# Kernel optimization log

Hardware: AMD Instinct MI355X
Metric: run time of the kernel (lower is better)

The kernel has to match this reference:

```python
import jax, jax.numpy as jnp
import numpy as np
from jax import lax

N, C, H, W = 64, 96, 18, 32
S_IN = 320          # input_state_size
HEADS, HD = 4, 96 // 4
HID = 96            # HIDDEN_SIZE
ENC = 320           # ENC_SIZE
K = 3               # KERNEL_SIZE


def _conv(x, k, b):
    y = lax.conv_general_dilated(x, k, (1, 1), 'SAME',
                                 dimension_numbers=('NCHW', 'OIHW', 'NCHW'))
    return y + b[None, :, None, None]


def setup_inputs() -> dict:
    key = jax.random.key(0)
    ks = jax.random.split(key, 16)
    sc = 0.02
    inp = {
        'x': jax.random.normal(ks[0], (N, C, H, W), jnp.float32),
        'x_state': jax.random.normal(ks[1], (N, S_IN), jnp.float32),
        'actor_keys': jax.random.randint(ks[2], (N,), 0, N),
        'hidden_states': 0.1 * jax.random.normal(ks[3], (N, HID, H, W), jnp.float32),
        # modulation Linear(S_IN -> 2*C), bias init 0
        'W_mod': sc * jax.random.normal(ks[4], (S_IN, 2 * C), jnp.float32),
        'b_mod': jnp.zeros((2 * C,), jnp.float32),
        # FiLM attention: qkv 1x1 proj and output proj
        'W_qkv': sc * jax.random.normal(ks[5], (C, 3 * C), jnp.float32),
        'b_qkv': jnp.zeros((3 * C,), jnp.float32),
        'W_proj': sc * jax.random.normal(ks[6], (C, C), jnp.float32),
        'b_proj': jnp.zeros((C,), jnp.float32),
        # IRConv2dCell (ConvGRU-style): gates conv (2C -> 2*HID), candidate conv (2C -> HID)
        'K_zr': sc * jax.random.normal(ks[7], (2 * HID, 2 * C, K, K), jnp.float32),
        'b_zr': jnp.zeros((2 * HID,), jnp.float32),
        'K_c': sc * jax.random.normal(ks[8], (HID, 2 * C, K, K), jnp.float32),
        'b_c': jnp.zeros((HID,), jnp.float32),
        # PosConv: learned positional map + 1x1 conv to ENC
        'pos_emb': sc * jax.random.normal(ks[9], (1, HID, H, W), jnp.float32),
        'W_pos': sc * jax.random.normal(ks[10], (ENC, HID), jnp.float32),
        'b_pos': jnp.zeros((ENC,), jnp.float32),
    }
    return inp


def reference(x, x_state, actor_keys, hidden_states,
              W_mod, b_mod, W_qkv, b_qkv, W_proj, b_proj,
              K_zr, b_zr, K_c, b_c, pos_emb, W_pos, b_pos):
    HW = H * W
    # modulation -> FiLM params
    mod = x_state @ W_mod + b_mod                       # [N, 2C]
    mm, mb = jnp.split(mod, 2, axis=1)                  # [N, C] each
    # FiLM-conditioned attention over spatial positions
    xm = x * mm[:, :, None, None] + mb[:, :, None, None]  # [N,C,H,W]
    xf = xm.reshape(N, C, HW).transpose(0, 2, 1)          # [N,HW,C]
    qkv = xf @ W_qkv + b_qkv                              # [N,HW,3C]
    q, k, v = jnp.split(qkv, 3, axis=-1)
    q = q.reshape(N, HW, HEADS, HD).transpose(0, 2, 1, 3)  # [N,h,HW,hd]
    k = k.reshape(N, HW, HEADS, HD).transpose(0, 2, 1, 3)
    v = v.reshape(N, HW, HEADS, HD).transpose(0, 2, 1, 3)
    attn = jax.nn.softmax(jnp.einsum('nhqd,nhkd->nhqk', q, k) / np.sqrt(HD), axis=-1)
    o = jnp.einsum('nhqk,nhkd->nhqd', attn, v)            # [N,h,HW,hd]
    o = o.transpose(0, 2, 1, 3).reshape(N, HW, C)
    o = o @ W_proj + b_proj
    y = x + o.transpose(0, 2, 1).reshape(N, C, H, W)      # residual
    # actor-keyed recurrent conv memory cell (gather per actor key)
    h = hidden_states[actor_keys]                         # [N,HID,H,W]
    xh = jnp.concatenate([y, h], axis=1)                  # [N,2C,H,W]
    zr = _conv(xh, K_zr, b_zr)
    z, r = jnp.split(jax.nn.sigmoid(zr), 2, axis=1)
    c = jnp.tanh(_conv(jnp.concatenate([y, r * h], axis=1), K_c, b_c))
    h_new = (1.0 - z) * h + z * c                         # [N,HID,H,W]
    # pooled outputs
    x_visual = h_new.reshape(N, HID, H // 2, 2, W // 2, 2).mean(axis=(3, 5))
    e = h_new + pos_emb
    enc = jnp.einsum('nchw,oc->nohw', e, W_pos) + b_pos[None, :, None, None]
    x_visual_enc = enc.max(axis=(2, 3))                   # [N,ENC]
    return (x_visual, x_visual_enc)
```

## Files before the change

### kernel.cpp

```cpp
#include <hip/hip_runtime.h>
#include <hip/hip_bf16.h>
#include <math.h>

#define NN 64
#define CC 96
#define HH 18
#define WW 32
#define HWP 576
#define SIN 320
#define NHEADS 4
#define HDIM 24
#define HIDC 96
#define ENCC 320

#define MOD_OFF   0
#define A_OFF     12288
#define Y_OFF     (A_OFF)
#define Z_OFF     (A_OFF + 3538944)
#define RH_OFF    (A_OFF + 7077888)
#define O_OFF     (A_OFF + 10616832)
#define HN_OFF    (O_OFF)
#define PART_OFF  (O_OFF + 3538944)
#define WTZR_OFF  (PART_OFF + 163840)
#define WTC_OFF   (WTZR_OFF + 165888)

typedef __attribute__((ext_vector_type(8))) short short8;
typedef __attribute__((ext_vector_type(4))) float f32x4;
typedef __attribute__((ext_vector_type(2))) unsigned int uint2v;
#define MFMA16(a, b, c) __builtin_amdgcn_mfma_f32_16x16x32_bf16(a, b, c, 0, 0, 0)

__device__ inline unsigned short f2bf(float f) {
  __hip_bfloat16 h = __float2bfloat16(f);
  return *reinterpret_cast<unsigned short*>(&h);
}
__device__ inline unsigned int cvtpk(float lo, float hi) {
  unsigned int r;
  asm volatile("v_cvt_pk_bf16_f32 %0, %1, %2" : "=v"(r) : "v"(lo), "v"(hi));
  return r;
}
union S8U { short8 s; unsigned int u[4]; };

__global__ __launch_bounds__(256) void k_modwt(const float* __restrict__ xs,
    const float* __restrict__ Wm, const float* __restrict__ bm,
    float* __restrict__ mod, const float* __restrict__ Kzr,
    const float* __restrict__ Kc, short* __restrict__ wz,
    short* __restrict__ wc) {
  __shared__ float s[SIN];
  int bid = blockIdx.x;
  if (bid < 64) {
    int n = bid;
    for (int i = threadIdx.x; i < SIN; i += 256) s[i] = xs[n * SIN + i];
    __syncthreads();
    int j = threadIdx.x;
    if (j < 192) {
      float acc = bm[j];
      #pragma unroll 4
      for (int k = 0; k < SIN; ++k) acc = fmaf(s[k], Wm[k * 192 + j], acc);
      mod[n * 192 + j] = acc;
    }
  } else {
    int idx = (bid - 64) * 256 + threadIdx.x;
    if (idx < 36864) {
      int oc = idx / 192, ic = idx % 192;
      const float* src = Kzr + (size_t)idx * 9;
      #pragma unroll
      for (int t = 0; t < 9; ++t)
        wz[(t * 192 + oc) * 192 + ic] = (short)f2bf(src[t]);
    } else {
      int j = idx - 36864;
      if (j < 18432) {
        int oc = j / 192, ic = j % 192;
        const float* src = Kc + (size_t)j * 9;
        #pragma unroll
        for (int t = 0; t < 9; ++t)
          wc[(t * 96 + oc) * 192 + ic] = (short)f2bf(src[t]);
      }
    }
  }
}

__global__ __launch_bounds__(256) void k_qkv(const float* __restrict__ x,
    const float* __restrict__ mod, const float* __restrict__ Wq,
    const float* __restrict__ bq, float* __restrict__ qkv) {
  int id = blockIdx.x;
  int n = id & 63, pt = id >> 6;
  int p0 = pt * 96;
  __shared__ __align__(16) short XT[96 * 104];
  int tid = threadIdx.x, lane = tid & 63, wid = tid >> 6;
  int wr = wid >> 1, wcn = wid & 1;
  int cl = lane & 15, kg = lane >> 4;
  #pragma unroll
  for (int w = 0; w < 9; ++w) {
    int lin = tid + 256 * w;
    int cp = lin / 48, pp = (lin % 48) * 2;
    float mA = mod[n * 192 + 2 * cp], bA = mod[n * 192 + 96 + 2 * cp];
    float mB = mod[n * 192 + 2 * cp + 1], bB = mod[n * 192 + 96 + 2 * cp + 1];
    float2 xa = *reinterpret_cast<const float2*>(
        &x[((size_t)n * CC + 2 * cp) * HWP + p0 + pp]);
    float2 xb = *reinterpret_cast<const float2*>(
        &x[((size_t)n * CC + 2 * cp + 1) * HWP + p0 + pp]);
    *reinterpret_cast<unsigned int*>(&XT[pp * 104 + 2 * cp]) =
        cvtpk(fmaf(xa.x, mA, bA), fmaf(xb.x, mB, bB));
    *reinterpret_cast<unsigned int*>(&XT[(pp + 1) * 104 + 2 * cp]) =
        cvtpk(fmaf(xa.y, mA, bA), fmaf(xb.y, mB, bB));
  }
  __syncthreads();

  f32x4 acc[3][9];
  #pragma unroll
  for (int mt = 0; mt < 3; ++mt)
    #pragma unroll
    for (int nt = 0; nt < 9; ++nt) acc[mt][nt] = (f32x4){0.f, 0.f, 0.f, 0.f};

  #pragma unroll
  for (int kc = 0; kc < 3; ++kc) {
    short8 af[3];
    #pragma unroll
    for (int mt = 0; mt < 3; ++mt) {
      int row = wr * 48 + mt * 16 + cl;
      af[mt] = *reinterpret_cast<const short8*>(
          &XT[row * 104 + kc * 32 + kg * 8]);
    }
    #pragma unroll
    for (int nt = 0; nt < 9; ++nt) {
      int j = wcn * 144 + nt * 16 + cl;
      const float* wp = Wq + (size_t)(kc * 32 + kg * 8) * 288 + j;
      S8U b;
      b.u[0] = cvtpk(wp[0], wp[288]);
      b.u[1] = cvtpk(wp[576], wp[864]);
      b.u[2] = cvtpk(wp[1152], wp[1440]);
      b.u[3] = cvtpk(wp[1728], wp[2016]);
      #pragma unroll
      for (int mt = 0; mt < 3; ++mt)
        acc[mt][nt] = MFMA16(af[mt], b.s, acc[mt][nt]);
    }
  }

  #pragma unroll
  for (int nt = 0; nt < 9; ++nt) {
    int j = wcn * 144 + nt * 16 + cl;
    float bias = bq[j];
    #pragma unroll
    for (int mt = 0; mt < 3; ++mt) {
      int pr = p0 + wr * 48 + mt * 16 + kg * 4;
      float* dst = qkv + ((size_t)n * HWP + pr) * 288 + j;
      dst[0] = acc[mt][nt][0] + bias;
      dst[288] = acc[mt][nt][1] + bias;
      dst[576] = acc[mt][nt][2] + bias;
      dst[864] = acc[mt][nt][3] + bias;
    }
  }
}

__global__ __launch_bounds__(256) void k_attn(const float* __restrict__ qkv,
                                              float* __restrict__ o) {
  int id = blockIdx.x;
  int n = id & 63, head = id >> 6;
  __shared__ __align__(16) short K_lds[576 * 40];
  __shared__ __align__(16) short VT_lds[24 * 584];
  __shared__ __align__(16) short P_lds[4 * 144 * 40];
  int tid = threadIdx.x, lane = tid & 63, wid = tid >> 6;
  int cl = lane & 15, kg = lane >> 4;
  const float* base = qkv + (size_t)n * HWP * 288;
  int qoff = head * HDIM, koff = CC + head * HDIM, voff = 2 * CC + head * HDIM;
  const float scale = 0.2041241452319315f;

  for (int p = tid; p < HWP; p += 256) {
    const float* ksrc = base + (size_t)p * 288 + koff;
    #pragma unroll
    for (int g = 0; g < 3; ++g) {
      float4 a = *(const float4*)(ksrc + g * 8);
      float4 b = *(const float4*)(ksrc + g * 8 + 4);
      S8U t;
      t.u[0] = cvtpk(a.x, a.y); t.u[1] = cvtpk(a.z, a.w);
      t.u[2] = cvtpk(b.x, b.y); t.u[3] = cvtpk(b.z, b.w);
      *reinterpret_cast<short8*>(&K_lds[p * 40 + g * 8]) = t.s;
    }
    *reinterpret_cast<short8*>(&K_lds[p * 40 + 24]) =
        (short8){0, 0, 0, 0, 0, 0, 0, 0};
    const float* vsrc = base + (size_t)p * 288 + voff;
    #pragma unroll
    for (int d = 0; d < HDIM; ++d) VT_lds[d * 584 + p] = (short)f2bf(vsrc[d]);
  }

  int qbase = wid * 144;
  short8 qf[9];
  #pragma unroll
  for (int qt = 0; qt < 9; ++qt) {
    if (kg < 3) {
      const float* qs =
          base + (size_t)(qbase + qt * 16 + cl) * 288 + qoff + kg * 8;
      float4 a = *(const float4*)qs;
      float4 b = *(const float4*)(qs + 4);
      S8U t;
      t.u[0] = cvtpk(a.x * scale, a.y * scale);
      t.u[1] = cvtpk(a.z * scale, a.w * scale);
      t.u[2] = cvtpk(b.x * scale, b.y * scale);
      t.u[3] = cvtpk(b.z * scale, b.w * scale);
      qf[qt] = t.s;
    } else {
      qf[qt] = (short8){0, 0, 0, 0, 0, 0, 0, 0};
    }
  }
  __syncthreads();

  f32x4 acc[9][2];
  float m[9], l[9];
  #pragma unroll
  for (int qt = 0; qt < 9; ++qt) {
    acc[qt][0] = (f32x4){0.f, 0.f, 0.f, 0.f};
    acc[qt][1] = (f32x4){0.f, 0.f, 0.f, 0.f};
    m[qt] = -1e30f; l[qt] = 0.f;
  }
  short* pw = P_lds + wid * 5760;
  const f32x4 z4 = (f32x4){0.f, 0.f, 0.f, 0.f};

  for (int ch = 0; ch < 18; ++ch) {
    int key0 = ch * 32;
    short8 ka0 = *reinterpret_cast<const short8*>(
        &K_lds[(key0 + cl) * 40 + kg * 8]);
    short8 ka1 = *reinterpret_cast<const short8*>(
        &K_lds[(key0 + 16 + cl) * 40 + kg * 8]);
    #pragma unroll
    for (int qt = 0; qt < 9; ++qt) {
      f32x4 s0 = MFMA16(ka0, qf[qt], z4);
      f32x4 s1 = MFMA16(ka1, qf[qt], z4);
      float mx = fmaxf(fmaxf(fmaxf(s0[0], s0[1]), fmaxf(s0[2], s0[3])),
                       fmaxf(fmaxf(s1[0], s1[1]), fmaxf(s1[2], s1[3])));
      mx = fmaxf(mx, __shfl_xor(mx, 16));
      mx = fmaxf(mx, __shfl_xor(mx, 32));
      float mn = fmaxf(m[qt], mx);
      float corr = __expf(m[qt] - mn);
      float p0 = __expf(s0[0] - mn), p1 = __expf(s0[1] - mn);
      float p2 = __expf(s0[2] - mn), p3 = __expf(s0[3] - mn);
      float p4 = __expf(s1[0] - mn), p5 = __expf(s1[1] - mn);
      float p6 = __expf(s1[2] - mn), p7 = __expf(s1[3] - mn);
      float sum = ((p0 + p1) + (p2 + p3)) + ((p4 + p5) + (p6 + p7));
      sum += __shfl_xor(sum, 16);
      sum += __shfl_xor(sum, 32);
      l[qt] = l[qt] * corr + sum;
      m[qt] = mn;
      float c0 = __shfl(corr, kg * 4 + 0);
      float c1 = __shfl(corr, kg * 4 + 1);
      float c2 = __shfl(corr, kg * 4 + 2);
      float c3 = __shfl(corr, kg * 4 + 3);
      acc[qt][0][0] *= c0; acc[qt][0][1] *= c1;
      acc[qt][0][2] *= c2; acc[qt][0][3] *= c3;
      acc[qt][1][0] *= c0; acc[qt][1][1] *= c1;
      acc[qt][1][2] *= c2; acc[qt][1][3] *= c3;
      uint2v w0 = {cvtpk(p0, p1), cvtpk(p2, p3)};
      uint2v w1 = {cvtpk(p4, p5), cvtpk(p6, p7)};
      short* prow = pw + (qt * 16 + cl) * 40;
      *reinterpret_cast<uint2v*>(&prow[4 * kg]) = w0;
      *reinterpret_cast<uint2v*>(&prow[16 + 4 * kg]) = w1;
    }
    short8 vb0 = *reinterpret_cast<const short8*>(
        &VT_lds[cl * 584 + key0 + kg * 8]);
    short8 vb1 = (cl < 8) ? *reinterpret_cast<const short8*>(
                                &VT_lds[(16 + cl) * 584 + key0 + kg * 8])
                          : (short8){0, 0, 0, 0, 0, 0, 0, 0};
    #pragma unroll
    for (int qt = 0; qt < 9; ++qt) {
      short8 pa = *reinterpret_cast<const short8*>(
          &pw[(qt * 16 + cl) * 40 + kg * 8]);
      acc[qt][0] = MFMA16(pa, vb0, acc[qt][0]);
      acc[qt][1] = MFMA16(pa, vb1, acc[qt][1]);
    }
  }

  #pragma unroll
  for (int qt = 0; qt < 9; ++qt) {
    float li0 = 1.f / __shfl(l[qt], kg * 4 + 0);
    float li1 = 1.f / __shfl(l[qt], kg * 4 + 1);
    float li2 = 1.f / __shfl(l[qt], kg * 4 + 2);
    float li3 = 1.f / __shfl(l[qt], kg * 4 + 3);
    #pragma unroll
    for (int dt = 0; dt < 2; ++dt) {
      int d = dt * 16 + cl;
      if (dt == 1 && cl >= 8) continue;
      size_t ob = ((size_t)n * HWP + qbase + qt * 16 + kg * 4) * CC
                  + head * HDIM + d;
      o[ob] = acc[qt][dt][0] * li0;
      o[ob + CC] = acc[qt][dt][1] * li1;
      o[ob + 2 * CC] = acc[qt][dt][2] * li2;
      o[ob + 3 * CC] = acc[qt][dt][3] * li3;
    }
  }
}

__global__ __launch_bounds__(256) void k_proj(const float* __restrict__ o,
    const float* __restrict__ Wp, const float* __restrict__ bp,
    const float* __restrict__ x, float* __restrict__ y) {
  int id = blockIdx.x;
  int n = id & 63, pt = id >> 6;
  int p0 = pt * 96;
  __shared__ __align__(16) short XT[96 * 104];
  int tid = threadIdx.x, lane = tid & 63, wid = tid >> 6;
  int wr = wid >> 1, wcn = wid & 1;
  int cl = lane & 15, kg = lane >> 4;
  #pragma unroll
  for (int w = 0; w < 9; ++w) {
    int lin = tid + 256 * w;
    int p = lin / 24, cg = lin % 24;
    float4 v = *reinterpret_cast<const float4*>(
        &o[((size_t)n * HWP + p0 + p) * CC + cg * 4]);
    uint2v u = {cvtpk(v.x, v.y), cvtpk(v.z, v.w)};
    *reinterpret_cast<uint2v*>(&XT[p * 104 + cg * 4]) = u;
  }
  __syncthreads();

  f32x4 acc[3][3];
  #pragma unroll
  for (int mt = 0; mt < 3; ++mt)
    #pragma unroll
    for (int nt = 0; nt < 3; ++nt) acc[mt][nt] = (f32x4){0.f, 0.f, 0.f, 0.f};

  #pragma unroll
  for (int kc = 0; kc < 3; ++kc) {
    short8 af[3];
    #pragma unroll
    for (int mt = 0; mt < 3; ++mt) {
      int row = wr * 48 + mt * 16 + cl;
      af[mt] = *reinterpret_cast<const short8*>(
          &XT[row * 104 + kc * 32 + kg * 8]);
    }
    #pragma unroll
    for (int nt = 0; nt < 3; ++nt) {
      int j = wcn * 48 + nt * 16 + cl;
      const float* wp = Wp + (size_t)(kc * 32 + kg * 8) * 96 + j;
      S8U b;
      b.u[0] = cvtpk(wp[0], wp[96]);
      b.u[1] = cvtpk(wp[192], wp[288]);
      b.u[2] = cvtpk(wp[384], wp[480]);
      b.u[3] = cvtpk(wp[576], wp[672]);
      #pragma unroll
      for (int mt = 0; mt < 3; ++mt)
        acc[mt][nt] = MFMA16(af[mt], b.s, acc[mt][nt]);
    }
  }

  #pragma unroll
  for (int nt = 0; nt < 3; ++nt) {
    int j = wcn * 48 + nt * 16 + cl;
    float bias = bp[j];
    #pragma unroll
    for (int mt = 0; mt < 3; ++mt) {
      int pr = p0 + wr * 48 + mt * 16 + kg * 4;
      size_t yi = ((size_t)n * CC + j) * HWP + pr;
      float4 xv = *reinterpret_cast<const float4*>(&x[yi]);
      float4 o4 = {xv.x + acc[mt][nt][0] + bias, xv.y + acc[mt][nt][1] + bias,
                   xv.z + acc[mt][nt][2] + bias, xv.w + acc[mt][nt][3] + bias};
      *reinterpret_cast<float4*>(&y[yi]) = o4;
    }
  }
}


__global__ __launch_bounds__(256) void k_conv_zr(const float* __restrict__ y,
    const float* __restrict__ hidden, const int* __restrict__ keys,
    const short* __restrict__ wt, const float* __restrict__ bb,
    float* __restrict__ z, float* __restrict__ rh) {
  int id = blockIdx.x;
  int n = id & 63, b = id >> 6;
  int bp = b % 6, bo = b / 6;
  int key = keys[n];
  int ocb = bo * 96;
  __shared__ __align__(16) short XT[170 * 68];
  int tid = threadIdx.x;
  int lane = tid & 63, wid = tid >> 6;
  int wr = wid >> 1, wc = wid & 1;
  int col = lane & 15, kg = lane >> 4;
  int icp = tid >> 4, psub = tid & 15;
  int pg0 = (3 * bp - 1) * 32;
  unsigned int* XTu = reinterpret_cast<unsigned int*>(XT);

  for (int i = tid; i < 5780; i += 256) XTu[i] = 0;

  f32x4 acc[3][3];
  #pragma unroll
  for (int m = 0; m < 3; ++m)
    #pragma unroll
    for (int nt = 0; nt < 3; ++nt) acc[m][nt] = (f32x4){0.f, 0.f, 0.f, 0.f};
  int rowm[3], pxm[3];
  #pragma unroll
  for (int m = 0; m < 3; ++m) {
    int pl = wr * 48 + m * 16 + col;
    rowm[m] = pl >> 5;
    pxm[m] = pl & 31;
  }
  int wl = (ocb + wc * 48 + col) * 192 + kg * 8;
  const float* hsrc = hidden + (size_t)key * HIDC * HWP;
  __syncthreads();

  #pragma unroll
  for (int ph = 0; ph < 3; ++ph) {
    #pragma unroll
    for (int c = 0; c < 2; ++c) {
      int gc = ph * 64 + c * 32;
      const float* s0 = (gc < 96)
          ? y + ((size_t)n * CC + gc + 2 * icp) * HWP
          : hsrc + (size_t)(gc - 96 + 2 * icp) * HWP;
      const float* s1 = s0 + HWP;
      #pragma unroll
      for (int j = 0; j < 5; ++j) {
        int pos = 32 * j + 2 * psub;
        int pg = pg0 + pos;
        bool ok = (pg >= 0 && pg < HWP);
        float2 a = ok ? *reinterpret_cast<const float2*>(s0 + pg)
                      : float2{0.f, 0.f};
        float2 bv = ok ? *reinterpret_cast<const float2*>(s1 + pg)
                       : float2{0.f, 0.f};
        int pidx0 = j * 34 + 1 + 2 * psub;
        XTu[pidx0 * 34 + c * 16 + icp] = cvtpk(a.x, bv.x);
        XTu[(pidx0 + 1) * 34 + c * 16 + icp] = cvtpk(a.y, bv.y);
      }
    }
    __syncthreads();
    #pragma unroll 3
    for (int t = 0; t < 9; ++t) {
      int dyp = t / 3, dxp = t % 3;
      const short* wci = wt + wl + t * 36864 + ph * 64;
      #pragma unroll
      for (int qc = 0; qc < 2; ++qc) {
        short8 b0 = *reinterpret_cast<const short8*>(wci + qc * 32);
        short8 b1 = *reinterpret_cast<const short8*>(wci + qc * 32 + 3072);
        short8 b2 = *reinterpret_cast<const short8*>(wci + qc * 32 + 6144);
        #pragma unroll
        for (int m = 0; m < 3; ++m) {
          int pidx = (rowm[m] + dyp) * 34 + pxm[m] + dxp;
          short8 a = *reinterpret_cast<const short8*>(
              XT + pidx * 68 + qc * 32 + kg * 8);
          acc[m][0] = MFMA16(a, b0, acc[m][0]);
          acc[m][1] = MFMA16(a, b1, acc[m][1]);
          acc[m][2] = MFMA16(a, b2, acc[m][2]);
        }
      }
    }
    __syncthreads();
  }

  #pragma unroll
  for (int nt = 0; nt < 3; ++nt) {
    int oc = ocb + wc * 48 + nt * 16 + col;
    float bias = bb[oc];
    #pragma unroll
    for (int m = 0; m < 3; ++m) {
      int p0 = bp * 96 + wr * 48 + m * 16 + kg * 4;
      f32x4 v = acc[m][nt];
      float e0 = 1.f / (1.f + __expf(-(v[0] + bias)));
      float e1 = 1.f / (1.f + __expf(-(v[1] + bias)));
      float e2 = 1.f / (1.f + __expf(-(v[2] + bias)));
      float e3 = 1.f / (1.f + __expf(-(v[3] + bias)));
      if (oc < CC) {
        float4 o4 = {e0, e1, e2, e3};
        *reinterpret_cast<float4*>(&z[((size_t)n * CC + oc) * HWP + p0]) = o4;
      } else {
        int c2 = oc - CC;
        float4 h4 = *reinterpret_cast<const float4*>(
            &hidden[((size_t)key * HIDC + c2) * HWP + p0]);
        float4 o4 = {e0 * h4.x, e1 * h4.y, e2 * h4.z, e3 * h4.w};
        *reinterpret_cast<float4*>(&rh[((size_t)n * CC + c2) * HWP + p0]) = o4;
      }
    }
  }
}

__global__ __launch_bounds__(256) void k_conv_c(const float* __restrict__ y,
    const float* __restrict__ rh, const int* __restrict__ keys,
    const float* __restrict__ z, const float* __restrict__ hidden,
    const short* __restrict__ wt, const float* __restrict__ bb,
    float* __restrict__ hn) {
  int id = blockIdx.x;
  int n = id & 63, bp = id >> 6;
  int key = keys[n];
  __shared__ __align__(16) short XT[170 * 68];
  int tid = threadIdx.x;
  int lane = tid & 63, wid = tid >> 6;
  int wr = wid >> 1, wc = wid & 1;
  int col = lane & 15, kg = lane >> 4;
  int icp = tid >> 4, psub = tid & 15;
  int pg0 = (3 * bp - 1) * 32;
  unsigned int* XTu = reinterpret_cast<unsigned int*>(XT);

  for (int i = tid; i < 5780; i += 256) XTu[i] = 0;

  f32x4 acc[3][3];
  #pragma unroll
  for (int m = 0; m < 3; ++m)
    #pragma unroll
    for (int nt = 0; nt < 3; ++nt) acc[m][nt] = (f32x4){0.f, 0.f, 0.f, 0.f};
  int rowm[3], pxm[3];
  #pragma unroll
  for (int m = 0; m < 3; ++m) {
    int pl = wr * 48 + m * 16 + col;
    rowm[m] = pl >> 5;
    pxm[m] = pl & 31;
  }
  int wl = (wc * 48 + col) * 192 + kg * 8;
  const float* rsrc = rh + (size_t)n * CC * HWP;
  __syncthreads();

  #pragma unroll
  for (int ph = 0; ph < 3; ++ph) {
    #pragma unroll
    for (int c = 0; c < 2; ++c) {
      int gc = ph * 64 + c * 32;
      const float* s0 = (gc < 96)
          ? y + ((size_t)n * CC + gc + 2 * icp) * HWP
          : rsrc + (size_t)(gc - 96 + 2 * icp) * HWP;
      const float* s1 = s0 + HWP;
      #pragma unroll
      for (int j = 0; j < 5; ++j) {
        int pos = 32 * j + 2 * psub;
        int pg = pg0 + pos;
        bool ok = (pg >= 0 && pg < HWP);
        float2 a = ok ? *reinterpret_cast<const float2*>(s0 + pg)
                      : float2{0.f, 0.f};
        float2 bv = ok ? *reinterpret_cast<const float2*>(s1 + pg)
                       : float2{0.f, 0.f};
        int pidx0 = j * 34 + 1 + 2 * psub;
        XTu[pidx0 * 34 + c * 16 + icp] = cvtpk(a.x, bv.x);
        XTu[(pidx0 + 1) * 34 + c * 16 + icp] = cvtpk(a.y, bv.y);
      }
    }
    __syncthreads();
    #pragma unroll 3
    for (int t = 0; t < 9; ++t) {
      int dyp = t / 3, dxp = t % 3;
      const short* wci = wt + wl + t * 18432 + ph * 64;
      #pragma unroll
      for (int qc = 0; qc < 2; ++qc) {
        short8 b0 = *reinterpret_cast<const short8*>(wci + qc * 32);
        short8 b1 = *reinterpret_cast<const short8*>(wci + qc * 32 + 3072);
        short8 b2 = *reinterpret_cast<const short8*>(wci + qc * 32 + 6144);
        #pragma unroll
        for (int m = 0; m < 3; ++m) {
          int pidx = (rowm[m] + dyp) * 34 + pxm[m] + dxp;
          short8 a = *reinterpret_cast<const short8*>(
              XT + pidx * 68 + qc * 32 + kg * 8);
          acc[m][0] = MFMA16(a, b0, acc[m][0]);
          acc[m][1] = MFMA16(a, b1, acc[m][1]);
          acc[m][2] = MFMA16(a, b2, acc[m][2]);
        }
      }
    }
    __syncthreads();
  }

  #pragma unroll
  for (int nt = 0; nt < 3; ++nt) {
    int oc = wc * 48 + nt * 16 + col;
    float bias = bb[oc];
    #pragma unroll
    for (int m = 0; m < 3; ++m) {
      int p0 = bp * 96 + wr * 48 + m * 16 + kg * 4;
      f32x4 v = acc[m][nt];
      float c0 = tanhf(v[0] + bias);
      float c1 = tanhf(v[1] + bias);
      float c2v = tanhf(v[2] + bias);
      float c3 = tanhf(v[3] + bias);
      float4 z4 = *reinterpret_cast<const float4*>(
          &z[((size_t)n * CC + oc) * HWP + p0]);
      float4 h4 = *reinterpret_cast<const float4*>(
          &hidden[((size_t)key * HIDC + oc) * HWP + p0]);
      float4 o4 = {(1.f - z4.x) * h4.x + z4.x * c0,
                   (1.f - z4.y) * h4.y + z4.y * c1,
                   (1.f - z4.z) * h4.z + z4.z * c2v,
                   (1.f - z4.w) * h4.w + z4.w * c3};
      *reinterpret_cast<float4*>(&hn[((size_t)n * CC + oc) * HWP + p0]) = o4;
    }
  }
}

__global__ __launch_bounds__(256) void k_enc(const float* __restrict__ hn,
    const float* __restrict__ pos, const float* __restrict__ Wp,
    float* __restrict__ part, float* __restrict__ out) {
  int id = blockIdx.x;
  int n = id & 63, pt = id >> 6;
  int p0 = pt * 96;
  __shared__ __align__(16) short XT[96 * 104];
  int tid = threadIdx.x, lane = tid & 63, wid = tid >> 6;
  int wr = wid >> 1, wcn = wid & 1;
  int cl = lane & 15, kg = lane >> 4;

  #pragma unroll
  for (int r = 0; r < 9; ++r) {
    int idx = id * 2304 + r * 256 + tid;
    int jj = idx & 15, ii = (idx >> 4) % 9, nc = idx / 144;
    const float* bsrc = hn + (size_t)nc * HWP + (2 * ii) * WW + 2 * jj;
    out[idx] = 0.25f * (bsrc[0] + bsrc[1] + bsrc[WW] + bsrc[WW + 1]);
  }

  #pragma unroll
  for (int w = 0; w < 9; ++w) {
    int lin = tid + 256 * w;
    int cp = lin / 48, pp = (lin % 48) * 2;
    float2 ha = *reinterpret_cast<const float2*>(
        &hn[((size_t)n * CC + 2 * cp) * HWP + p0 + pp]);
    float2 hb = *reinterpret_cast<const float2*>(
        &hn[((size_t)n * CC + 2 * cp + 1) * HWP + p0 + pp]);
    float2 pa = *reinterpret_cast<const float2*>(&pos[(2 * cp) * HWP + p0 + pp]);
    float2 pc = *reinterpret_cast<const float2*>(
        &pos[(2 * cp + 1) * HWP + p0 + pp]);
    *reinterpret_cast<unsigned int*>(&XT[pp * 104 + 2 * cp]) =
        cvtpk(ha.x + pa.x, hb.x + pc.x);
    *reinterpret_cast<unsigned int*>(&XT[(pp + 1) * 104 + 2 * cp]) =
        cvtpk(ha.y + pa.y, hb.y + pc.y);
  }
  __syncthreads();

  f32x4 acc[3][10];
  #pragma unroll
  for (int mt = 0; mt < 3; ++mt)
    #pragma unroll
    for (int nt = 0; nt < 10; ++nt) acc[mt][nt] = (f32x4){0.f, 0.f, 0.f, 0.f};

  #pragma unroll
  for (int kc = 0; kc < 3; ++kc) {
    short8 af[3];
    #pragma unroll
    for (int mt = 0; mt < 3; ++mt) {
      int row = wr * 48 + mt * 16 + cl;
      af[mt] = *reinterpret_cast<const short8*>(
          &XT[row * 104 + kc * 32 + kg * 8]);
    }
    #pragma unroll
    for (int nt = 0; nt < 10; ++nt) {
      int oc = wcn * 160 + nt * 16 + cl;
      const float* wp = Wp + (size_t)oc * CC + kc * 32 + kg * 8;
      float4 w0 = *reinterpret_cast<const float4*>(wp);
      float4 w1 = *reinterpret_cast<const float4*>(wp + 4);
      S8U b;
      b.u[0] = cvtpk(w0.x, w0.y); b.u[1] = cvtpk(w0.z, w0.w);
      b.u[2] = cvtpk(w1.x, w1.y); b.u[3] = cvtpk(w1.z, w1.w);
      #pragma unroll
      for (int mt = 0; mt < 3; ++mt)
        acc[mt][nt] = MFMA16(af[mt], b.s, acc[mt][nt]);
    }
  }

  #pragma unroll
  for (int nt = 0; nt < 10; ++nt) {
    float mx = -1e30f;
    #pragma unroll
    for (int mt = 0; mt < 3; ++mt) {
      mx = fmaxf(mx, fmaxf(fmaxf(acc[mt][nt][0], acc[mt][nt][1]),
                           fmaxf(acc[mt][nt][2], acc[mt][nt][3])));
    }
    mx = fmaxf(mx, __shfl_xor(mx, 16));
    mx = fmaxf(mx, __shfl_xor(mx, 32));
    if (kg == 0) {
      int oc = wcn * 160 + nt * 16 + cl;
      part[(((size_t)n * 6 + pt) * 2 + wr) * ENCC + oc] = mx;
    }
  }
}

__global__ __launch_bounds__(320) void k_reduce(const float* __restrict__ part,
    const float* __restrict__ bpos, float* __restrict__ out) {
  int n = blockIdx.x, o = threadIdx.x;
  float mx = -1e30f;
  #pragma unroll
  for (int t = 0; t < 12; ++t)
    mx = fmaxf(mx, part[((size_t)n * 12 + t) * ENCC + o]);
  out[NN * CC * 144 + n * ENCC + o] = mx + bpos[o];
}

extern "C" void kernel_launch(void* const* d_in, const int* in_sizes, int n_in,
                              void* d_out, int out_size, void* d_ws, size_t ws_size,
                              hipStream_t stream) {
  const float* x       = (const float*)d_in[0];
  const float* x_state = (const float*)d_in[1];
  const int*   keys    = (const int*)d_in[2];
  const float* hidden  = (const float*)d_in[3];
  const float* W_mod   = (const float*)d_in[4];
  const float* b_mod   = (const float*)d_in[5];
  const float* W_qkv   = (const float*)d_in[6];
  const float* b_qkv   = (const float*)d_in[7];
  const float* W_proj  = (const float*)d_in[8];
  const float* b_proj  = (const float*)d_in[9];
  const float* K_zr    = (const float*)d_in[10];
  const float* b_zr    = (const float*)d_in[11];
  const float* K_c     = (const float*)d_in[12];
  const float* b_c     = (const float*)d_in[13];
  const float* pos_emb = (const float*)d_in[14];
  const float* W_pos   = (const float*)d_in[15];
  const float* b_pos   = (const float*)d_in[16];
  float* out = (float*)d_out;
  float* ws  = (float*)d_ws;
  short* wtzr = (short*)(ws + WTZR_OFF);
  short* wtc  = (short*)(ws + WTC_OFF);

  k_modwt<<<280, 256, 0, stream>>>(x_state, W_mod, b_mod, ws + MOD_OFF,
                                   K_zr, K_c, wtzr, wtc);
  k_qkv<<<384, 256, 0, stream>>>(x, ws + MOD_OFF, W_qkv, b_qkv, ws + A_OFF);
  k_attn<<<256, 256, 0, stream>>>(ws + A_OFF, ws + O_OFF);
  k_proj<<<384, 256, 0, stream>>>(ws + O_OFF, W_proj, b_proj, x, ws + Y_OFF);
  k_conv_zr<<<768, 256, 0, stream>>>(ws + Y_OFF, hidden, keys, wtzr, b_zr,
                                     ws + Z_OFF, ws + RH_OFF);
  k_conv_c<<<384, 256, 0, stream>>>(ws + Y_OFF, ws + RH_OFF, keys, ws + Z_OFF,
                                    hidden, wtc, b_c, ws + HN_OFF);
  k_enc<<<384, 256, 0, stream>>>(ws + HN_OFF, pos_emb, W_pos, ws + PART_OFF,
                                 out);
  k_reduce<<<NN, 320, 0, stream>>>(ws + PART_OFF, b_pos, out);
}
```

Baseline: 292.3 us.

## Split output-column halves across blocks instead of waves in four GEMM kernels

After: 296.3 us. No clear change (+1.4%).

```diff
diff --git a/kernel.cpp b/kernel.cpp
--- a/kernel.cpp
+++ b/kernel.cpp
@@ -79,19 +79,19 @@
   }
 }
 
-__global__ __launch_bounds__(256) void k_qkv(const float* __restrict__ x,
+__global__ __launch_bounds__(128) void k_qkv(const float* __restrict__ x,
     const float* __restrict__ mod, const float* __restrict__ Wq,
     const float* __restrict__ bq, float* __restrict__ qkv) {
   int id = blockIdx.x;
-  int n = id & 63, pt = id >> 6;
+  int n = id & 63, rem = id >> 6;
+  int pt = rem % 6, jh = rem / 6;
   int p0 = pt * 96;
   __shared__ __align__(16) short XT[96 * 104];
-  int tid = threadIdx.x, lane = tid & 63, wid = tid >> 6;
-  int wr = wid >> 1, wcn = wid & 1;
+  int tid = threadIdx.x, lane = tid & 63, wr = tid >> 6;
   int cl = lane & 15, kg = lane >> 4;
   #pragma unroll
-  for (int w = 0; w < 9; ++w) {
-    int lin = tid + 256 * w;
+  for (int w = 0; w < 18; ++w) {
+    int lin = tid + 128 * w;
     int cp = lin / 48, pp = (lin % 48) * 2;
     float mA = mod[n * 192 + 2 * cp], bA = mod[n * 192 + 96 + 2 * cp];
     float mB = mod[n * 192 + 2 * cp + 1], bB = mod[n * 192 + 96 + 2 * cp + 1];
@@ -123,7 +123,7 @@
     }
     #pragma unroll
     for (int nt = 0; nt < 9; ++nt) {
-      int j = wcn * 144 + nt * 16 + cl;
+      int j = jh * 144 + nt * 16 + cl;
       const float* wp = Wq + (size_t)(kc * 32 + kg * 8) * 288 + j;
       S8U b;
       b.u[0] = cvtpk(wp[0], wp[288]);
@@ -138,7 +138,7 @@
 
   #pragma unroll
   for (int nt = 0; nt < 9; ++nt) {
-    int j = wcn * 144 + nt * 16 + cl;
+    int j = jh * 144 + nt * 16 + cl;
     float bias = bq[j];
     #pragma unroll
     for (int mt = 0; mt < 3; ++mt) {
@@ -288,19 +288,19 @@
   }
 }
 
-__global__ __launch_bounds__(256) void k_proj(const float* __restrict__ o,
+__global__ __launch_bounds__(128) void k_proj(const float* __restrict__ o,
     const float* __restrict__ Wp, const float* __restrict__ bp,
     const float* __restrict__ x, float* __restrict__ y) {
   int id = blockIdx.x;
-  int n = id & 63, pt = id >> 6;
+  int n = id & 63, rem = id >> 6;
+  int pt = rem % 6, jh = rem / 6;
   int p0 = pt * 96;
   __shared__ __align__(16) short XT[96 * 104];
-  int tid = threadIdx.x, lane = tid & 63, wid = tid >> 6;
-  int wr = wid >> 1, wcn = wid & 1;
+  int tid = threadIdx.x, lane = tid & 63, wr = tid >> 6;
   int cl = lane & 15, kg = lane >> 4;
   #pragma unroll
-  for (int w = 0; w < 9; ++w) {
-    int lin = tid + 256 * w;
+  for (int w = 0; w < 18; ++w) {
+    int lin = tid + 128 * w;
     int p = lin / 24, cg = lin % 24;
     float4 v = *reinterpret_cast<const float4*>(
         &o[((size_t)n * HWP + p0 + p) * CC + cg * 4]);
@@ -326,7 +326,7 @@
     }
     #pragma unroll
     for (int nt = 0; nt < 3; ++nt) {
-      int j = wcn * 48 + nt * 16 + cl;
+      int j = jh * 48 + nt * 16 + cl;
       const float* wp = Wp + (size_t)(kc * 32 + kg * 8) * 96 + j;
       S8U b;
       b.u[0] = cvtpk(wp[0], wp[96]);
@@ -341,7 +341,7 @@
 
   #pragma unroll
   for (int nt = 0; nt < 3; ++nt) {
-    int j = wcn * 48 + nt * 16 + cl;
+    int j = jh * 48 + nt * 16 + cl;
     float bias = bp[j];
     #pragma unroll
     for (int mt = 0; mt < 3; ++mt) {
@@ -465,24 +465,24 @@
   }
 }
 
-__global__ __launch_bounds__(256) void k_conv_c(const float* __restrict__ y,
+__global__ __launch_bounds__(128) void k_conv_c(const float* __restrict__ y,
     const float* __restrict__ rh, const int* __restrict__ keys,
     const float* __restrict__ z, const float* __restrict__ hidden,
     const short* __restrict__ wt, const float* __restrict__ bb,
     float* __restrict__ hn) {
   int id = blockIdx.x;
-  int n = id & 63, bp = id >> 6;
+  int n = id & 63, rem = id >> 6;
+  int bp = rem % 6, och = rem / 6;
   int key = keys[n];
   __shared__ __align__(16) short XT[170 * 68];
   int tid = threadIdx.x;
-  int lane = tid & 63, wid = tid >> 6;
-  int wr = wid >> 1, wc = wid & 1;
+  int lane = tid & 63, wr = tid >> 6;
   int col = lane & 15, kg = lane >> 4;
   int icp = tid >> 4, psub = tid & 15;
   int pg0 = (3 * bp - 1) * 32;
   unsigned int* XTu = reinterpret_cast<unsigned int*>(XT);
 
-  for (int i = tid; i < 5780; i += 256) XTu[i] = 0;
+  for (int i = tid; i < 5780; i += 128) XTu[i] = 0;
 
   f32x4 acc[3][3];
   #pragma unroll
@@ -496,15 +496,15 @@
     rowm[m] = pl >> 5;
     pxm[m] = pl & 31;
   }
-  int wl = (wc * 48 + col) * 192 + kg * 8;
+  int wl = (och * 48 + col) * 192 + kg * 8;
   const float* rsrc = rh + (size_t)n * CC * HWP;
   __syncthreads();
 
   #pragma unroll
   for (int ph = 0; ph < 3; ++ph) {
     #pragma unroll
-    for (int c = 0; c < 2; ++c) {
-      int gc = ph * 64 + c * 32;
+    for (int c = 0; c < 4; ++c) {
+      int gc = ph * 64 + c * 16;
       const float* s0 = (gc < 96)
           ? y + ((size_t)n * CC + gc + 2 * icp) * HWP
           : rsrc + (size_t)(gc - 96 + 2 * icp) * HWP;
@@ -519,8 +519,8 @@
         float2 bv = ok ? *reinterpret_cast<const float2*>(s1 + pg)
                        : float2{0.f, 0.f};
         int pidx0 = j * 34 + 1 + 2 * psub;
-        XTu[pidx0 * 34 + c * 16 + icp] = cvtpk(a.x, bv.x);
-        XTu[(pidx0 + 1) * 34 + c * 16 + icp] = cvtpk(a.y, bv.y);
+        XTu[pidx0 * 34 + c * 8 + icp] = cvtpk(a.x, bv.x);
+        XTu[(pidx0 + 1) * 34 + c * 8 + icp] = cvtpk(a.y, bv.y);
       }
     }
     __syncthreads();
@@ -549,7 +549,7 @@
 
   #pragma unroll
   for (int nt = 0; nt < 3; ++nt) {
-    int oc = wc * 48 + nt * 16 + col;
+    int oc = och * 48 + nt * 16 + col;
     float bias = bb[oc];
     #pragma unroll
     for (int m = 0; m < 3; ++m) {
@@ -572,28 +572,28 @@
   }
 }
 
-__global__ __launch_bounds__(256) void k_enc(const float* __restrict__ hn,
+__global__ __launch_bounds__(128) void k_enc(const float* __restrict__ hn,
     const float* __restrict__ pos, const float* __restrict__ Wp,
     float* __restrict__ part, float* __restrict__ out) {
   int id = blockIdx.x;
-  int n = id & 63, pt = id >> 6;
+  int n = id & 63, rem = id >> 6;
+  int pt = rem % 6, wcn = rem / 6;
   int p0 = pt * 96;
   __shared__ __align__(16) short XT[96 * 104];
-  int tid = threadIdx.x, lane = tid & 63, wid = tid >> 6;
-  int wr = wid >> 1, wcn = wid & 1;
+  int tid = threadIdx.x, lane = tid & 63, wr = tid >> 6;
   int cl = lane & 15, kg = lane >> 4;
 
   #pragma unroll
   for (int r = 0; r < 9; ++r) {
-    int idx = id * 2304 + r * 256 + tid;
+    int idx = id * 1152 + r * 128 + tid;
     int jj = idx & 15, ii = (idx >> 4) % 9, nc = idx / 144;
     const float* bsrc = hn + (size_t)nc * HWP + (2 * ii) * WW + 2 * jj;
     out[idx] = 0.25f * (bsrc[0] + bsrc[1] + bsrc[WW] + bsrc[WW + 1]);
   }
 
   #pragma unroll
-  for (int w = 0; w < 9; ++w) {
-    int lin = tid + 256 * w;
+  for (int w = 0; w < 18; ++w) {
+    int lin = tid + 128 * w;
     int cp = lin / 48, pp = (lin % 48) * 2;
     float2 ha = *reinterpret_cast<const float2*>(
         &hn[((size_t)n * CC + 2 * cp) * HWP + p0 + pp]);
@@ -693,14 +693,14 @@
 
   k_modwt<<<280, 256, 0, stream>>>(x_state, W_mod, b_mod, ws + MOD_OFF,
                                    K_zr, K_c, wtzr, wtc);
-  k_qkv<<<384, 256, 0, stream>>>(x, ws + MOD_OFF, W_qkv, b_qkv, ws + A_OFF);
+  k_qkv<<<768, 128, 0, stream>>>(x, ws + MOD_OFF, W_qkv, b_qkv, ws + A_OFF);
   k_attn<<<256, 256, 0, stream>>>(ws + A_OFF, ws + O_OFF);
-  k_proj<<<384, 256, 0, stream>>>(ws + O_OFF, W_proj, b_proj, x, ws + Y_OFF);
+  k_proj<<<768, 128, 0, stream>>>(ws + O_OFF, W_proj, b_proj, x, ws + Y_OFF);
   k_conv_zr<<<768, 256, 0, stream>>>(ws + Y_OFF, hidden, keys, wtzr, b_zr,
                                      ws + Z_OFF, ws + RH_OFF);
-  k_conv_c<<<384, 256, 0, stream>>>(ws + Y_OFF, ws + RH_OFF, keys, ws + Z_OFF,
+  k_conv_c<<<768, 128, 0, stream>>>(ws + Y_OFF, ws + RH_OFF, keys, ws + Z_OFF,
                                     hidden, wtc, b_c, ws + HN_OFF);
-  k_enc<<<384, 256, 0, stream>>>(ws + HN_OFF, pos_emb, W_pos, ws + PART_OFF,
+  k_enc<<<768, 128, 0, stream>>>(ws + HN_OFF, pos_emb, W_pos, ws + PART_OFF,
                                  out);
   k_reduce<<<NN, 320, 0, stream>>>(ws + PART_OFF, b_pos, out);
 }
```
